# Optimization experiments

Measured on AMD Instinct MI355X. Metric: run time of the kernel, lower is better.

## Reference

```python
import jax, jax.numpy as jnp
import numpy as np

T = 32        # time_step
H = 64        # n_hidden (and dense width)
A = 8         # nb_actions
OBS_DIM = 512
B = 4096      # sequences; obs rows = B*T
LN_EPS = 1e-12  # tf.contrib.layers.layer_norm epsilon


def setup_inputs() -> dict:
    key = jax.random.key(0)
    ks = jax.random.split(key, 10)
    s = 0.1
    return {
        "obs":  jax.random.normal(ks[0], (B * T, OBS_DIM), jnp.float32),
        "W0":   jax.random.normal(ks[1], (OBS_DIM, H), jnp.float32) * s,
        "b0":   jnp.zeros((H,), jnp.float32),
        "gamma": jnp.ones((H,), jnp.float32),
        "beta":  jnp.zeros((H,), jnp.float32),
        "Wfw":  jax.random.normal(ks[2], (2 * H, 4 * H), jnp.float32) * s,
        "bfw":  jnp.zeros((4 * H,), jnp.float32),
        "Wbw":  jax.random.normal(ks[3], (2 * H, 4 * H), jnp.float32) * s,
        "bbw":  jnp.zeros((4 * H,), jnp.float32),
        "Wc":   jax.random.uniform(ks[4], (H, A), jnp.float32, -0.003, 0.003),
        "bc":   jnp.zeros((A,), jnp.float32),
    }


def _lstm_scan(xs, W, b):
    """BasicLSTMCell (forget_bias=1.0). xs: [T, B, H] -> hs: [T, B, H]."""
    nb = xs.shape[1]
    init = (jnp.zeros((nb, H), xs.dtype), jnp.zeros((nb, H), xs.dtype))

    def step(carry, x_t):
        c, h = carry
        z = jnp.concatenate([x_t, h], axis=-1) @ W + b  # [B, 4H]
        i, j, f, o = jnp.split(z, 4, axis=-1)           # TF gate order i,j,f,o
        c = c * jax.nn.sigmoid(f + 1.0) + jax.nn.sigmoid(i) * jnp.tanh(j)
        h = jnp.tanh(c) * jax.nn.sigmoid(o)
        return (c, h), h

    _, hs = jax.lax.scan(step, init, xs)
    return hs


def reference(obs, W0, b0, gamma, beta, Wfw, bfw, Wbw, bbw, Wc, bc):
    # dense(64) + layer_norm + relu
    x = obs @ W0 + b0                                   # [B*T, H]
    mu = jnp.mean(x, axis=-1, keepdims=True)
    var = jnp.mean(jnp.square(x - mu), axis=-1, keepdims=True)
    x = gamma * (x - mu) / jnp.sqrt(var + LN_EPS) + beta
    x = jax.nn.relu(x)

    xt = x.reshape(-1, T, H).transpose(1, 0, 2)          # [T, B, H]
    hs_fw = _lstm_scan(xt, Wfw, bfw)                     # [T, B, H]
    hs_bw = _lstm_scan(xt[::-1], Wbw, bbw)[::-1]         # reverse-in, reverse-out

    # tf.reshape on the (fw, bw) tuple stacks along a new leading axis:
    # [2, B, T, H] -> [2B, T*H, 1]; conv1d(kernel=stride=H) == per-step proj.
    y = jnp.stack([hs_fw.transpose(1, 0, 2), hs_bw.transpose(1, 0, 2)], axis=0)
    y = y.reshape(-1, T, H)                              # [2B, T, H]
    out = jnp.tanh(jnp.einsum('btk,ka->bta', y, Wc) + bc)  # [2B, T, A]
    return out
```

## Files before the change

### kernel.cpp

```cpp
#include <hip/hip_runtime.h>
#include <hip/hip_bf16.h>

typedef __attribute__((ext_vector_type(8))) short bf16x8;
typedef __attribute__((ext_vector_type(4))) float f32x4;

#define MFMA_BF16 __builtin_amdgcn_mfma_f32_16x16x32_bf16

#define GLDS16(gp, lp)                                                        \
  __builtin_amdgcn_global_load_lds(                                           \
      (const __attribute__((address_space(1))) void*)(gp),                    \
      (__attribute__((address_space(3))) void*)(lp), 16, 0, 0)

__device__ __forceinline__ unsigned pk2(float a, float b) {
  __hip_bfloat162 t = __float22bfloat162_rn(make_float2(a, b));
  return *reinterpret_cast<unsigned*>(&t);
}
__device__ __forceinline__ unsigned short f2bf_hw(float f) {
  __hip_bfloat16 h = __float2bfloat16(f);
  return *reinterpret_cast<unsigned short*>(&h);
}

__global__ void k0_conv(const float* __restrict__ W0, const float* __restrict__ Wfw,
                        const float* __restrict__ Wbw, unsigned short* __restrict__ wfrag,
                        unsigned short* __restrict__ wlstm) {
  int gid = blockIdx.x * 256 + threadIdx.x;
  if (gid < 4096) {
    int f = gid >> 6, l = gid & 63;
    int k0 = (f >> 2) * 32 + ((l >> 4) << 3);
    int n = (f & 3) * 16 + (l & 15);
    bf16x8 v;
#pragma unroll
    for (int j = 0; j < 8; ++j) v[j] = (short)f2bf_hw(W0[(k0 + j) * 64 + n]);
    *(bf16x8*)(wfrag + gid * 8) = v;
  } else if (gid < 12288) {
    int g2 = gid - 4096;
    const float* W = (g2 < 4096) ? Wfw : Wbw;
    int f = (g2 & 4095) >> 6, l = g2 & 63;
    int wv = f >> 4, gate = (f >> 2) & 3, kf = f & 3;
    int col = gate * 64 + wv * 16 + (l & 15);
    int kr = kf * 32 + ((l >> 4) << 3);
    bf16x8 v;
#pragma unroll
    for (int j = 0; j < 8; ++j) v[j] = (short)f2bf_hw(W[(kr + j) * 256 + col]);
    *(bf16x8*)(wlstm + g2 * 8) = v;
  }
}

__global__ __launch_bounds__(256, 3) void k_dense_ln(
    const float* __restrict__ obs, const unsigned short* __restrict__ wfrag,
    const float* __restrict__ b0, const float* __restrict__ gam,
    const float* __restrict__ bet, unsigned short* __restrict__ xout) {
  __shared__ __align__(16) char lds[49152];
  const int tid = threadIdx.x, w = tid >> 6, l = tid & 63;
  const int g = l >> 4, c = l & 15;
  const long blk64 = (long)blockIdx.x * 64;
  const long rb = blk64 + w * 16;

  float b0v[4], gv[4], bv[4];
#pragma unroll
  for (int nt = 0; nt < 4; ++nt) {
    int col = nt * 16 + c;
    b0v[nt] = b0[col]; gv[nt] = gam[col]; bv[nt] = bet[col];
  }
  const unsigned short* wfl = wfrag + l * 8;
  const char* gB = (const char*)obs + blk64 * 2048;

  const int rlo = w * 4 + g;
  asm volatile("s_waitcnt vmcnt(0)" ::: "memory");

#define K1_STAGE(q)                                                           \
  {                                                                           \
    _Pragma("unroll") for (int i = 0; i < 4; ++i) {                           \
      int row_ = i * 16 + rlo;                                                \
      const char* gp_ = gB + (long)row_ * 2048 + (q) * 256 +                  \
                        (long)((c ^ rlo) * 16);                               \
      char* lp_ = lds + ((q) % 3) * 16384 + (i * 4096 + (w * 64 + l) * 16);   \
      GLDS16(gp_, lp_);                                                       \
    }                                                                         \
  }

  K1_STAGE(0);
  K1_STAGE(1);
  K1_STAGE(2);

  f32x4 acc[4];
#pragma unroll
  for (int nt = 0; nt < 4; ++nt) acc[nt] = (f32x4){0.f, 0.f, 0.f, 0.f};

#pragma unroll
  for (int q = 0; q < 8; ++q) {
    constexpr int VW[8] = {8, 16, 24, 24, 24, 24, 20, 16};
    asm volatile("s_waitcnt vmcnt(%0)" :: "i"(VW[q]) : "memory");
    __builtin_amdgcn_s_barrier();
    __builtin_amdgcn_sched_barrier(0);

    const char* rowb = lds + (q % 3) * 16384 + (w * 16 + c) * 256;
#pragma unroll
    for (int kf = 0; kf < 2; ++kf) {
      int fb = (q * 2 + kf) * 4;
      bf16x8 B0 = *(const bf16x8*)(wfl + (fb + 0) * 512);
      bf16x8 B1 = *(const bf16x8*)(wfl + (fb + 1) * 512);
      bf16x8 B2 = *(const bf16x8*)(wfl + (fb + 2) * 512);
      bf16x8 B3 = *(const bf16x8*)(wfl + (fb + 3) * 512);
      int u0 = kf * 8 + g * 2;
      float4 f0 = *(const float4*)(rowb + ((u0 + 0) ^ c) * 16);
      float4 f1 = *(const float4*)(rowb + ((u0 + 1) ^ c) * 16);
      union { bf16x8 v; unsigned u[4]; } af;
      af.u[0] = pk2(f0.x, f0.y); af.u[1] = pk2(f0.z, f0.w);
      af.u[2] = pk2(f1.x, f1.y); af.u[3] = pk2(f1.z, f1.w);
      acc[0] = MFMA_BF16(af.v, B0, acc[0], 0, 0, 0);
      acc[1] = MFMA_BF16(af.v, B1, acc[1], 0, 0, 0);
      acc[2] = MFMA_BF16(af.v, B2, acc[2], 0, 0, 0);
      acc[3] = MFMA_BF16(af.v, B3, acc[3], 0, 0, 0);
    }
    if (q < 5) {
      __builtin_amdgcn_s_barrier();
      __builtin_amdgcn_sched_barrier(0);
      K1_STAGE(q + 3);
    }
  }

  float vv[4][4], s1[4], s2[4];
#pragma unroll
  for (int r = 0; r < 4; ++r) { s1[r] = 0.f; s2[r] = 0.f; }
#pragma unroll
  for (int nt = 0; nt < 4; ++nt)
#pragma unroll
    for (int r = 0; r < 4; ++r) {
      float val = acc[nt][r] + b0v[nt];
      vv[nt][r] = val; s1[r] += val; s2[r] += val * val;
    }
#pragma unroll
  for (int r = 0; r < 4; ++r) {
#pragma unroll
    for (int m = 1; m <= 8; m <<= 1) {
      s1[r] += __shfl_xor(s1[r], m);
      s2[r] += __shfl_xor(s2[r], m);
    }
  }
  unsigned short* xw = (unsigned short*)lds + w * 1024;
#pragma unroll
  for (int r = 0; r < 4; ++r) {
    float mu = s1[r] * 0.015625f;
    float var = s2[r] * 0.015625f - mu * mu;
    float inv = rsqrtf(var + 1e-12f);
    int row = g * 4 + r;
#pragma unroll
    for (int nt = 0; nt < 4; ++nt) {
      float xn = (vv[nt][r] - mu) * inv * gv[nt] + bv[nt];
      xw[(row * 64 + nt * 16 + c) ^ (g << 3)] = f2bf_hw(fmaxf(xn, 0.f));
    }
  }
#pragma unroll
  for (int m2 = 0; m2 < 2; ++m2) {
    int m = m2 * 64 + l;
    int row = m >> 3, u8 = m & 7;
    bf16x8 v = *(const bf16x8*)(xw + ((row * 64 + u8 * 8) ^ ((row >> 2) << 3)));
    *(bf16x8*)(xout + (rb + row) * 64 + u8 * 8) = v;
  }
}

__global__ __launch_bounds__(256, 2) void k_lstm(
    const unsigned short* __restrict__ x, const unsigned short* __restrict__ wlstm,
    const float* __restrict__ bfw, const float* __restrict__ bbw,
    const float* __restrict__ Wc, const float* __restrict__ bc,
    float* __restrict__ out) {
  __shared__ __align__(16) char xl[65536];
  __shared__ unsigned short hl[2 * 1024];
  const int tid = threadIdx.x, w = tid >> 6, l = tid & 63;
  const int g = l >> 4, c = l & 15;
  const int dir = blockIdx.x >> 8;
  const int sq = (blockIdx.x & 255) * 16;
  const float* bias = dir ? bbw : bfw;

  bf16x8 Bf[4][4];
  const unsigned short* wl = wlstm + ((long)dir * 4096 + w * 16 * 64) * 8;
#pragma unroll
  for (int gate = 0; gate < 4; ++gate)
#pragma unroll
    for (int kf = 0; kf < 4; ++kf)
      Bf[gate][kf] = *(const bf16x8*)(wl + ((gate * 4 + kf) * 64 + l) * 8);
  float bz[4];
#pragma unroll
  for (int gate = 0; gate < 4; ++gate) bz[gate] = bias[gate * 64 + w * 16 + c];

  bf16x8 Pc[2];
#pragma unroll
  for (int kf = 0; kf < 2; ++kf)
#pragma unroll
    for (int j = 0; j < 8; ++j) Pc[kf][j] = 0;
  float bcv = 0.f;
  if (w == 0 && c < 8) {
#pragma unroll
    for (int kf = 0; kf < 2; ++kf)
#pragma unroll
      for (int j = 0; j < 8; ++j)
        Pc[kf][j] = (short)f2bf_hw(Wc[(kf * 32 + g * 8 + j) * 8 + c]);
    bcv = bc[c];
  }

  asm volatile("s_waitcnt vmcnt(0)" ::: "memory");

  const int ss = l >> 3, sc = l & 7;
#pragma unroll
  for (int j = 0; j < 8; ++j) {
    int tt = w * 8 + j;
    int te = dir ? 31 - tt : tt;
#pragma unroll
    for (int p = 0; p < 2; ++p) {
      int s = p * 8 + ss;
      const char* gp = (const char*)x +
          ((long)(sq + s) * 32 + te) * 128 + (long)(sc ^ (s & 7)) * 16;
      char* lp = xl + tt * 2048 + p * 1024;
      GLDS16(gp, lp);
    }
  }

  for (int i = tid; i < 1024; i += 256) ((unsigned*)hl)[i] = 0u;
  float cs[4] = {0.f, 0.f, 0.f, 0.f};

  if (w == 0) asm volatile("s_waitcnt vmcnt(12)" ::: "memory");
  asm volatile("s_waitcnt lgkmcnt(0)" ::: "memory");
  __builtin_amdgcn_s_barrier();
  __builtin_amdgcn_sched_barrier(0);

  const int hq = w >> 1;
  const int hgp = ((w & 1) * 2 + (c >> 3)) * 16;
  const int hlo = c & 7;

  f32x4 accx[4];
  {
    const char* xt = xl + 0 * 2048 + c * 128;
    bf16x8 Ax0 = *(const bf16x8*)(xt + (long)((g) ^ (c & 7)) * 16);
    bf16x8 Ax1 = *(const bf16x8*)(xt + (long)((4 + g) ^ (c & 7)) * 16);
#pragma unroll
    for (int gate = 0; gate < 4; ++gate) {
      f32x4 b = (f32x4){bz[gate], bz[gate], bz[gate], bz[gate]};
      accx[gate] = MFMA_BF16(Ax1, Bf[gate][1],
                             MFMA_BF16(Ax0, Bf[gate][0], b, 0, 0, 0), 0, 0, 0);
    }
  }

  int p = 0;
#pragma unroll
  for (int t = 0; t < 32; ++t) {
    bf16x8 Ah0 = *(const bf16x8*)((const char*)hl + p * 2048 + l * 16);
    bf16x8 Ah1 = *(const bf16x8*)((const char*)hl + p * 2048 + 1024 + l * 16);

    f32x4 acc[4];
#pragma unroll
    for (int gate = 0; gate < 4; ++gate)
      acc[gate] = MFMA_BF16(Ah1, Bf[gate][3],
                            MFMA_BF16(Ah0, Bf[gate][2], accx[gate], 0, 0, 0),
                            0, 0, 0);

    if (t + 1 < 32) {
      const char* xt = xl + (t + 1) * 2048 + c * 128;
      bf16x8 Ax0 = *(const bf16x8*)(xt + (long)((g) ^ (c & 7)) * 16);
      bf16x8 Ax1 = *(const bf16x8*)(xt + (long)((4 + g) ^ (c & 7)) * 16);
#pragma unroll
      for (int gate = 0; gate < 4; ++gate) {
        f32x4 b = (f32x4){bz[gate], bz[gate], bz[gate], bz[gate]};
        accx[gate] = MFMA_BF16(Ax1, Bf[gate][1],
                               MFMA_BF16(Ax0, Bf[gate][0], b, 0, 0, 0), 0, 0, 0);
      }
    }

    const int wb = (p ^ 1) * 1024;
#pragma unroll
    for (int r = 0; r < 4; ++r) {
      float ei = __expf(-acc[0][r]);
      float ej = __expf(2.f * acc[1][r]);
      float ef = __expf(-(acc[2][r] + 1.f));
      float eo = __expf(-acc[3][r]);
      float p12 = (1.f + ei) * (1.f + ej);
      float r3 = __builtin_amdgcn_rcpf(p12 * (1.f + ef));
      float it = (ej - 1.f) * (1.f + ef) * r3;
      float sf = p12 * r3;
      cs[r] = cs[r] * sf + it;
      float ec = __expf(2.f * cs[r]);
      float r2 = __builtin_amdgcn_rcpf((1.f + eo) * (1.f + ec));
      hl[wb + (hq * 64 + hgp + 4 * g + r) * 8 + hlo] =
          f2bf_hw((ec - 1.f) * r2);
    }

    if (t + 2 < 32) {
      if (w == ((t + 2) >> 3))
        asm volatile("s_waitcnt vmcnt(%0)" :: "i"(14 - 2 * ((t + 2) & 7)) : "memory");
    }
    asm volatile("s_waitcnt lgkmcnt(0)" ::: "memory");
    __builtin_amdgcn_s_barrier();
    __builtin_amdgcn_sched_barrier(0);

    if (w == 0 && t >= 1) {
      int te = dir ? 31 - t : t;
      f32x4 pa = (f32x4){0.f, 0.f, 0.f, 0.f};
      pa = MFMA_BF16(Ah0, Pc[0], pa, 0, 0, 0);
      pa = MFMA_BF16(Ah1, Pc[1], pa, 0, 0, 0);
      if (c < 8) {
        int tp = dir ? 32 - t : t - 1;
#pragma unroll
        for (int r = 0; r < 4; ++r) {
          long orow = (long)dir * 4096 + sq + 4 * g + r;
          out[(orow * 32 + tp) * 8 + c] = tanhf(pa[r] + bcv);
        }
      }
    }
    p ^= 1;
  }

  if (w == 0) {
    bf16x8 Ph0 = *(const bf16x8*)((const char*)hl + p * 2048 + l * 16);
    bf16x8 Ph1 = *(const bf16x8*)((const char*)hl + p * 2048 + 1024 + l * 16);
    f32x4 pa = (f32x4){0.f, 0.f, 0.f, 0.f};
    pa = MFMA_BF16(Ph0, Pc[0], pa, 0, 0, 0);
    pa = MFMA_BF16(Ph1, Pc[1], pa, 0, 0, 0);
    if (c < 8) {
      int tp = dir ? 0 : 31;
#pragma unroll
      for (int r = 0; r < 4; ++r) {
        long orow = (long)dir * 4096 + sq + 4 * g + r;
        out[(orow * 32 + tp) * 8 + c] = tanhf(pa[r] + bcv);
      }
    }
  }
}

extern "C" void kernel_launch(void* const* d_in, const int* in_sizes, int n_in,
                              void* d_out, int out_size, void* d_ws, size_t ws_size,
                              hipStream_t stream) {
  const float* obs = (const float*)d_in[0];
  const float* W0  = (const float*)d_in[1];
  const float* b0  = (const float*)d_in[2];
  const float* gam = (const float*)d_in[3];
  const float* bet = (const float*)d_in[4];
  const float* Wfw = (const float*)d_in[5];
  const float* bfw = (const float*)d_in[6];
  const float* Wbw = (const float*)d_in[7];
  const float* bbw = (const float*)d_in[8];
  const float* Wc  = (const float*)d_in[9];
  const float* bc  = (const float*)d_in[10];
  float* out = (float*)d_out;

  unsigned short* wfrag = (unsigned short*)d_ws;
  unsigned short* wlstm = wfrag + 4096 * 8;
  unsigned short* xbf   = wlstm + 8192 * 8;

  k0_conv<<<48, 256, 0, stream>>>(W0, Wfw, Wbw, wfrag, wlstm);
  k_dense_ln<<<2048, 256, 0, stream>>>(obs, wfrag, b0, gam, bet, xbf);
  k_lstm<<<512, 256, 0, stream>>>(xbf, wlstm, bfw, bbw, Wc, bc, out);
}
```

Measured before the change: 102.3 us.

## Ring-buffer LSTM input staging, spread output projection across warps, coalesce output stores

Replaces the 64KB all-timesteps LDS buffer with an 8-slot ring buffer that is refilled during the time loop by a rotating warp. This cuts LDS use and may raise occupancy. The per-step output projection now runs on all four warps, each handling one row group, and uses a fast exp-based tanh. Results are gathered in an LDS tile and written to global memory at the end with coalesced float4 stores. Partial unrolling and the in-loop prefetch add sync dependencies, and the vmcnt accounting becomes fragile.

```diff
diff --git a/kernel.cpp b/kernel.cpp
--- a/kernel.cpp
+++ b/kernel.cpp
@@ -18,6 +18,9 @@
 __device__ __forceinline__ unsigned short f2bf_hw(float f) {
   __hip_bfloat16 h = __float2bfloat16(f);
   return *reinterpret_cast<unsigned short*>(&h);
+}
+__device__ __forceinline__ float tanh_f(float x) {
+  return 1.f - 2.f * __builtin_amdgcn_rcpf(1.f + __expf(2.f * x));
 }
 
 __global__ void k0_conv(const float* __restrict__ W0, const float* __restrict__ Wfw,
@@ -165,8 +168,9 @@
     const float* __restrict__ bfw, const float* __restrict__ bbw,
     const float* __restrict__ Wc, const float* __restrict__ bc,
     float* __restrict__ out) {
-  __shared__ __align__(16) char xl[65536];
+  __shared__ __align__(16) char xr[8 * 2048];
   __shared__ unsigned short hl[2 * 1024];
+  __shared__ float pl[16 * 32 * 8];
   const int tid = threadIdx.x, w = tid >> 6, l = tid & 63;
   const int g = l >> 4, c = l & 15;
   const int dir = blockIdx.x >> 8;
@@ -190,7 +194,7 @@
 #pragma unroll
     for (int j = 0; j < 8; ++j) Pc[kf][j] = 0;
   float bcv = 0.f;
-  if (w == 0 && c < 8) {
+  if (c < 8) {
 #pragma unroll
     for (int kf = 0; kf < 2; ++kf)
 #pragma unroll
@@ -202,24 +206,25 @@
   asm volatile("s_waitcnt vmcnt(0)" ::: "memory");
 
   const int ss = l >> 3, sc = l & 7;
-#pragma unroll
-  for (int j = 0; j < 8; ++j) {
-    int tt = w * 8 + j;
-    int te = dir ? 31 - tt : tt;
-#pragma unroll
-    for (int p = 0; p < 2; ++p) {
-      int s = p * 8 + ss;
-      const char* gp = (const char*)x +
-          ((long)(sq + s) * 32 + te) * 128 + (long)(sc ^ (s & 7)) * 16;
-      char* lp = xl + tt * 2048 + p * 1024;
-      GLDS16(gp, lp);
-    }
-  }
+#define K2_STAGE(tt)                                                          \
+  {                                                                           \
+    int te_ = dir ? 31 - (tt) : (tt);                                         \
+    _Pragma("unroll") for (int p_ = 0; p_ < 2; ++p_) {                        \
+      int s_ = p_ * 8 + ss;                                                   \
+      const char* gp_ = (const char*)x +                                      \
+          ((long)(sq + s_) * 32 + te_) * 128 + (long)(sc ^ (s_ & 7)) * 16;    \
+      char* lp_ = xr + ((tt) & 7) * 2048 + p_ * 1024;                         \
+      GLDS16(gp_, lp_);                                                       \
+    }                                                                         \
+  }
+
+  K2_STAGE(w);
+  K2_STAGE(w + 4);
 
   for (int i = tid; i < 1024; i += 256) ((unsigned*)hl)[i] = 0u;
   float cs[4] = {0.f, 0.f, 0.f, 0.f};
 
-  if (w == 0) asm volatile("s_waitcnt vmcnt(12)" ::: "memory");
+  if (w < 2) asm volatile("s_waitcnt vmcnt(2)" ::: "memory");
   asm volatile("s_waitcnt lgkmcnt(0)" ::: "memory");
   __builtin_amdgcn_s_barrier();
   __builtin_amdgcn_sched_barrier(0);
@@ -230,7 +235,7 @@
 
   f32x4 accx[4];
   {
-    const char* xt = xl + 0 * 2048 + c * 128;
+    const char* xt = xr + c * 128;
     bf16x8 Ax0 = *(const bf16x8*)(xt + (long)((g) ^ (c & 7)) * 16);
     bf16x8 Ax1 = *(const bf16x8*)(xt + (long)((4 + g) ^ (c & 7)) * 16);
 #pragma unroll
@@ -242,7 +247,7 @@
   }
 
   int p = 0;
-#pragma unroll
+#pragma unroll 2
   for (int t = 0; t < 32; ++t) {
     bf16x8 Ah0 = *(const bf16x8*)((const char*)hl + p * 2048 + l * 16);
     bf16x8 Ah1 = *(const bf16x8*)((const char*)hl + p * 2048 + 1024 + l * 16);
@@ -255,7 +260,7 @@
                             0, 0, 0);
 
     if (t + 1 < 32) {
-      const char* xt = xl + (t + 1) * 2048 + c * 128;
+      const char* xt = xr + ((t + 1) & 7) * 2048 + c * 128;
       bf16x8 Ax0 = *(const bf16x8*)(xt + (long)((g) ^ (c & 7)) * 16);
       bf16x8 Ax1 = *(const bf16x8*)(xt + (long)((4 + g) ^ (c & 7)) * 16);
 #pragma unroll
@@ -280,49 +285,54 @@
       cs[r] = cs[r] * sf + it;
       float ec = __expf(2.f * cs[r]);
       float r2 = __builtin_amdgcn_rcpf((1.f + eo) * (1.f + ec));
-      hl[wb + (hq * 64 + hgp + 4 * g + r) * 8 + hlo] =
-          f2bf_hw((ec - 1.f) * r2);
-    }
-
-    if (t + 2 < 32) {
-      if (w == ((t + 2) >> 3))
-        asm volatile("s_waitcnt vmcnt(%0)" :: "i"(14 - 2 * ((t + 2) & 7)) : "memory");
-    }
+      hl[wb + (hq * 64 + hgp + 4 * g + r) * 8 + hlo] = f2bf_hw((ec - 1.f) * r2);
+    }
+
+    if (t + 8 < 32 && w == (t & 3)) K2_STAGE(t + 8);
+
+    if (t + 2 < 32 && w == ((t + 2) & 3))
+      asm volatile("s_waitcnt vmcnt(2)" ::: "memory");
     asm volatile("s_waitcnt lgkmcnt(0)" ::: "memory");
     __builtin_amdgcn_s_barrier();
     __builtin_amdgcn_sched_barrier(0);
 
-    if (w == 0 && t >= 1) {
-      int te = dir ? 31 - t : t;
+    if (t >= 1) {
       f32x4 pa = (f32x4){0.f, 0.f, 0.f, 0.f};
       pa = MFMA_BF16(Ah0, Pc[0], pa, 0, 0, 0);
       pa = MFMA_BF16(Ah1, Pc[1], pa, 0, 0, 0);
-      if (c < 8) {
+      if (g == w && c < 8) {
         int tp = dir ? 32 - t : t - 1;
 #pragma unroll
-        for (int r = 0; r < 4; ++r) {
-          long orow = (long)dir * 4096 + sq + 4 * g + r;
-          out[(orow * 32 + tp) * 8 + c] = tanhf(pa[r] + bcv);
-        }
+        for (int r = 0; r < 4; ++r)
+          pl[(4 * g + r) * 256 + tp * 8 + c] = tanh_f(pa[r] + bcv);
       }
     }
     p ^= 1;
   }
 
-  if (w == 0) {
+  {
     bf16x8 Ph0 = *(const bf16x8*)((const char*)hl + p * 2048 + l * 16);
     bf16x8 Ph1 = *(const bf16x8*)((const char*)hl + p * 2048 + 1024 + l * 16);
     f32x4 pa = (f32x4){0.f, 0.f, 0.f, 0.f};
     pa = MFMA_BF16(Ph0, Pc[0], pa, 0, 0, 0);
     pa = MFMA_BF16(Ph1, Pc[1], pa, 0, 0, 0);
-    if (c < 8) {
+    if (g == w && c < 8) {
       int tp = dir ? 0 : 31;
 #pragma unroll
-      for (int r = 0; r < 4; ++r) {
-        long orow = (long)dir * 4096 + sq + 4 * g + r;
-        out[(orow * 32 + tp) * 8 + c] = tanhf(pa[r] + bcv);
-      }
-    }
+      for (int r = 0; r < 4; ++r)
+        pl[(4 * g + r) * 256 + tp * 8 + c] = tanh_f(pa[r] + bcv);
+    }
+  }
+
+  asm volatile("s_waitcnt lgkmcnt(0)" ::: "memory");
+  __builtin_amdgcn_s_barrier();
+#pragma unroll
+  for (int i = 0; i < 4; ++i) {
+    int fi = tid + i * 256;
+    int s = fi >> 6, rem = fi & 63;
+    int t2 = rem >> 1, a4 = (rem & 1) * 4;
+    float4 v = *(const float4*)(pl + s * 256 + t2 * 8 + a4);
+    *(float4*)(out + ((long)(dir * 4096 + sq + s) * 32 + t2) * 8 + a4) = v;
   }
 }
 
```

New measurement: 104.1 us. About the same (+1.8%).

## Process two 64-row tiles per block in dense+layernorm kernel with continuous pipeline

Applied to the files above, without the earlier changes.

The dense+LN kernel now handles two consecutive 64-row tiles per workgroup, with half as many blocks. The triple-buffered LDS load pipeline runs across both tiles without draining between them, and tile-0 results are kept in registers until the end. This removes one pipeline fill/drain per tile and halves the per-block setup cost. In exchange it uses more registers for the held results and there are fewer blocks to spread across the CUs. It also adds an unused sigmoid helper and removes a dead variable in the LSTM kernel.

```diff
diff --git a/kernel.cpp b/kernel.cpp
--- a/kernel.cpp
+++ b/kernel.cpp
@@ -18,6 +18,9 @@
 __device__ __forceinline__ unsigned short f2bf_hw(float f) {
   __hip_bfloat16 h = __float2bfloat16(f);
   return *reinterpret_cast<unsigned short*>(&h);
+}
+__device__ __forceinline__ float sigm(float x) {
+  return __builtin_amdgcn_rcpf(1.f + __expf(-x));
 }
 
 __global__ void k0_conv(const float* __restrict__ W0, const float* __restrict__ Wfw,
@@ -53,8 +56,6 @@
   __shared__ __align__(16) char lds[49152];
   const int tid = threadIdx.x, w = tid >> 6, l = tid & 63;
   const int g = l >> 4, c = l & 15;
-  const long blk64 = (long)blockIdx.x * 64;
-  const long rb = blk64 + w * 16;
 
   float b0v[4], gv[4], bv[4];
 #pragma unroll
@@ -63,18 +64,18 @@
     b0v[nt] = b0[col]; gv[nt] = gam[col]; bv[nt] = bet[col];
   }
   const unsigned short* wfl = wfrag + l * 8;
-  const char* gB = (const char*)obs + blk64 * 2048;
-
+  const char* gB = (const char*)obs + (long)blockIdx.x * 262144;
   const int rlo = w * 4 + g;
+
   asm volatile("s_waitcnt vmcnt(0)" ::: "memory");
 
-#define K1_STAGE(q)                                                           \
+#define K1_STAGE(cc)                                                          \
   {                                                                           \
     _Pragma("unroll") for (int i = 0; i < 4; ++i) {                           \
       int row_ = i * 16 + rlo;                                                \
-      const char* gp_ = gB + (long)row_ * 2048 + (q) * 256 +                  \
-                        (long)((c ^ rlo) * 16);                               \
-      char* lp_ = lds + ((q) % 3) * 16384 + (i * 4096 + (w * 64 + l) * 16);   \
+      const char* gp_ = gB + ((cc) >> 3) * 131072 + (long)row_ * 2048 +       \
+                        ((cc) & 7) * 256 + (long)((c ^ rlo) * 16);            \
+      char* lp_ = lds + ((cc) % 3) * 16384 + (i * 4096 + (w * 64 + l) * 16);  \
       GLDS16(gp_, lp_);                                                       \
     }                                                                         \
   }
@@ -86,18 +87,20 @@
   f32x4 acc[4];
 #pragma unroll
   for (int nt = 0; nt < 4; ++nt) acc[nt] = (f32x4){0.f, 0.f, 0.f, 0.f};
-
-#pragma unroll
-  for (int q = 0; q < 8; ++q) {
-    constexpr int VW[8] = {8, 16, 24, 24, 24, 24, 20, 16};
-    asm volatile("s_waitcnt vmcnt(%0)" :: "i"(VW[q]) : "memory");
+  unsigned short hv[2][16];
+
+#pragma unroll
+  for (int qq = 0; qq < 16; ++qq) {
+    constexpr int VW[16] = {8, 16, 24, 24, 24, 24, 24, 24,
+                            24, 24, 24, 24, 24, 24, 20, 16};
+    asm volatile("s_waitcnt vmcnt(%0)" :: "i"(VW[qq]) : "memory");
     __builtin_amdgcn_s_barrier();
     __builtin_amdgcn_sched_barrier(0);
 
-    const char* rowb = lds + (q % 3) * 16384 + (w * 16 + c) * 256;
+    const char* rowb = lds + (qq % 3) * 16384 + (w * 16 + c) * 256;
 #pragma unroll
     for (int kf = 0; kf < 2; ++kf) {
-      int fb = (q * 2 + kf) * 4;
+      int fb = ((qq & 7) * 2 + kf) * 4;
       bf16x8 B0 = *(const bf16x8*)(wfl + (fb + 0) * 512);
       bf16x8 B1 = *(const bf16x8*)(wfl + (fb + 1) * 512);
       bf16x8 B2 = *(const bf16x8*)(wfl + (fb + 2) * 512);
@@ -113,50 +116,65 @@
       acc[2] = MFMA_BF16(af.v, B2, acc[2], 0, 0, 0);
       acc[3] = MFMA_BF16(af.v, B3, acc[3], 0, 0, 0);
     }
-    if (q < 5) {
+    if (qq < 13) {
       __builtin_amdgcn_s_barrier();
       __builtin_amdgcn_sched_barrier(0);
-      K1_STAGE(q + 3);
-    }
-  }
-
-  float vv[4][4], s1[4], s2[4];
-#pragma unroll
-  for (int r = 0; r < 4; ++r) { s1[r] = 0.f; s2[r] = 0.f; }
-#pragma unroll
-  for (int nt = 0; nt < 4; ++nt)
+      K1_STAGE(qq + 3);
+    }
+    if ((qq & 7) == 7) {
+      const int tile = qq >> 3;
+      float vv[4][4], s1[4], s2[4];
+#pragma unroll
+      for (int r = 0; r < 4; ++r) { s1[r] = 0.f; s2[r] = 0.f; }
+#pragma unroll
+      for (int nt = 0; nt < 4; ++nt)
+#pragma unroll
+        for (int r = 0; r < 4; ++r) {
+          float val = acc[nt][r] + b0v[nt];
+          vv[nt][r] = val; s1[r] += val; s2[r] += val * val;
+        }
+#pragma unroll
+      for (int r = 0; r < 4; ++r) {
+#pragma unroll
+        for (int m = 1; m <= 8; m <<= 1) {
+          s1[r] += __shfl_xor(s1[r], m);
+          s2[r] += __shfl_xor(s2[r], m);
+        }
+      }
+#pragma unroll
+      for (int r = 0; r < 4; ++r) {
+        float mu = s1[r] * 0.015625f;
+        float var = s2[r] * 0.015625f - mu * mu;
+        float inv = rsqrtf(var + 1e-12f);
+#pragma unroll
+        for (int nt = 0; nt < 4; ++nt) {
+          float xn = (vv[nt][r] - mu) * inv * gv[nt] + bv[nt];
+          hv[tile][r * 4 + nt] = f2bf_hw(fmaxf(xn, 0.f));
+        }
+      }
+#pragma unroll
+      for (int nt = 0; nt < 4; ++nt) acc[nt] = (f32x4){0.f, 0.f, 0.f, 0.f};
+    }
+  }
+
+  unsigned short* xw = (unsigned short*)(lds + 16384) + w * 1024;
+#pragma unroll
+  for (int tile = 0; tile < 2; ++tile) {
+    const long rbt = ((long)blockIdx.x * 2 + tile) * 64 + w * 16;
 #pragma unroll
     for (int r = 0; r < 4; ++r) {
-      float val = acc[nt][r] + b0v[nt];
-      vv[nt][r] = val; s1[r] += val; s2[r] += val * val;
-    }
-#pragma unroll
-  for (int r = 0; r < 4; ++r) {
-#pragma unroll
-    for (int m = 1; m <= 8; m <<= 1) {
-      s1[r] += __shfl_xor(s1[r], m);
-      s2[r] += __shfl_xor(s2[r], m);
-    }
-  }
-  unsigned short* xw = (unsigned short*)lds + w * 1024;
-#pragma unroll
-  for (int r = 0; r < 4; ++r) {
-    float mu = s1[r] * 0.015625f;
-    float var = s2[r] * 0.015625f - mu * mu;
-    float inv = rsqrtf(var + 1e-12f);
-    int row = g * 4 + r;
-#pragma unroll
-    for (int nt = 0; nt < 4; ++nt) {
-      float xn = (vv[nt][r] - mu) * inv * gv[nt] + bv[nt];
-      xw[(row * 64 + nt * 16 + c) ^ (g << 3)] = f2bf_hw(fmaxf(xn, 0.f));
-    }
-  }
-#pragma unroll
-  for (int m2 = 0; m2 < 2; ++m2) {
-    int m = m2 * 64 + l;
-    int row = m >> 3, u8 = m & 7;
-    bf16x8 v = *(const bf16x8*)(xw + ((row * 64 + u8 * 8) ^ ((row >> 2) << 3)));
-    *(bf16x8*)(xout + (rb + row) * 64 + u8 * 8) = v;
+      int row = g * 4 + r;
+#pragma unroll
+      for (int nt = 0; nt < 4; ++nt)
+        xw[(row * 64 + nt * 16 + c) ^ (g << 3)] = hv[tile][r * 4 + nt];
+    }
+#pragma unroll
+    for (int m2 = 0; m2 < 2; ++m2) {
+      int m = m2 * 64 + l;
+      int row = m >> 3, u8 = m & 7;
+      bf16x8 v = *(const bf16x8*)(xw + ((row * 64 + u8 * 8) ^ ((row >> 2) << 3)));
+      *(bf16x8*)(xout + (rbt + row) * 64 + u8 * 8) = v;
+    }
   }
 }
 
@@ -280,8 +298,7 @@
       cs[r] = cs[r] * sf + it;
       float ec = __expf(2.f * cs[r]);
       float r2 = __builtin_amdgcn_rcpf((1.f + eo) * (1.f + ec));
-      hl[wb + (hq * 64 + hgp + 4 * g + r) * 8 + hlo] =
-          f2bf_hw((ec - 1.f) * r2);
+      hl[wb + (hq * 64 + hgp + 4 * g + r) * 8 + hlo] = f2bf_hw((ec - 1.f) * r2);
     }
 
     if (t + 2 < 32) {
@@ -293,7 +310,6 @@
     __builtin_amdgcn_sched_barrier(0);
 
     if (w == 0 && t >= 1) {
-      int te = dir ? 31 - t : t;
       f32x4 pa = (f32x4){0.f, 0.f, 0.f, 0.f};
       pa = MFMA_BF16(Ah0, Pc[0], pa, 0, 0, 0);
       pa = MFMA_BF16(Ah1, Pc[1], pa, 0, 0, 0);
@@ -347,6 +363,6 @@
   unsigned short* xbf   = wlstm + 8192 * 8;
 
   k0_conv<<<48, 256, 0, stream>>>(W0, Wfw, Wbw, wfrag, wlstm);
-  k_dense_ln<<<2048, 256, 0, stream>>>(obs, wfrag, b0, gam, bet, xbf);
+  k_dense_ln<<<1024, 256, 0, stream>>>(obs, wfrag, b0, gam, bet, xbf);
   k_lstm<<<512, 256, 0, stream>>>(xbf, wlstm, bfw, bbw, Wc, bc, out);
 }
```

New measurement: 112.3 us. +9.8%, slower.

## Defer output projection to after the recurrence, storing h into the consumed x buffer

Applied to the files above, without the earlier changes.

Each step's hidden state is now also written into that step's slot of the LDS x buffer, which the recurrence has already consumed. The per-step projection that wave 0 ran inside the serial loop is removed. After the loop all waves compute the projection and output for their own 8 time steps, using a cheaper exp/rcp tanh. This takes work off the serial critical path and spreads it across waves, at the cost of an extra LDS store per step and an added barrier before the loop so the x buffer is fully read before it is overwritten.

```diff
diff --git a/kernel.cpp b/kernel.cpp
--- a/kernel.cpp
+++ b/kernel.cpp
@@ -18,6 +18,9 @@
 __device__ __forceinline__ unsigned short f2bf_hw(float f) {
   __hip_bfloat16 h = __float2bfloat16(f);
   return *reinterpret_cast<unsigned short*>(&h);
+}
+__device__ __forceinline__ float tanh_f(float x) {
+  return 1.f - 2.f * __builtin_amdgcn_rcpf(1.f + __expf(2.f * x));
 }
 
 __global__ void k0_conv(const float* __restrict__ W0, const float* __restrict__ Wfw,
@@ -190,7 +193,7 @@
 #pragma unroll
     for (int j = 0; j < 8; ++j) Pc[kf][j] = 0;
   float bcv = 0.f;
-  if (w == 0 && c < 8) {
+  if (c < 8) {
 #pragma unroll
     for (int kf = 0; kf < 2; ++kf)
 #pragma unroll
@@ -240,6 +243,9 @@
                              MFMA_BF16(Ax0, Bf[gate][0], b, 0, 0, 0), 0, 0, 0);
     }
   }
+  asm volatile("s_waitcnt lgkmcnt(0)" ::: "memory");
+  __builtin_amdgcn_s_barrier();
+  __builtin_amdgcn_sched_barrier(0);
 
   int p = 0;
 #pragma unroll
@@ -267,6 +273,7 @@
     }
 
     const int wb = (p ^ 1) * 1024;
+    unsigned short* xh = (unsigned short*)xl + t * 1024;
 #pragma unroll
     for (int r = 0; r < 4; ++r) {
       float ei = __expf(-acc[0][r]);
@@ -280,8 +287,10 @@
       cs[r] = cs[r] * sf + it;
       float ec = __expf(2.f * cs[r]);
       float r2 = __builtin_amdgcn_rcpf((1.f + eo) * (1.f + ec));
-      hl[wb + (hq * 64 + hgp + 4 * g + r) * 8 + hlo] =
-          f2bf_hw((ec - 1.f) * r2);
+      unsigned short hb = f2bf_hw((ec - 1.f) * r2);
+      int off = (hq * 64 + hgp + 4 * g + r) * 8 + hlo;
+      hl[wb + off] = hb;
+      xh[off] = hb;
     }
 
     if (t + 2 < 32) {
@@ -291,36 +300,24 @@
     asm volatile("s_waitcnt lgkmcnt(0)" ::: "memory");
     __builtin_amdgcn_s_barrier();
     __builtin_amdgcn_sched_barrier(0);
-
-    if (w == 0 && t >= 1) {
-      int te = dir ? 31 - t : t;
-      f32x4 pa = (f32x4){0.f, 0.f, 0.f, 0.f};
-      pa = MFMA_BF16(Ah0, Pc[0], pa, 0, 0, 0);
-      pa = MFMA_BF16(Ah1, Pc[1], pa, 0, 0, 0);
-      if (c < 8) {
-        int tp = dir ? 32 - t : t - 1;
-#pragma unroll
-        for (int r = 0; r < 4; ++r) {
-          long orow = (long)dir * 4096 + sq + 4 * g + r;
-          out[(orow * 32 + tp) * 8 + c] = tanhf(pa[r] + bcv);
-        }
-      }
-    }
     p ^= 1;
   }
 
-  if (w == 0) {
-    bf16x8 Ph0 = *(const bf16x8*)((const char*)hl + p * 2048 + l * 16);
-    bf16x8 Ph1 = *(const bf16x8*)((const char*)hl + p * 2048 + 1024 + l * 16);
+#pragma unroll
+  for (int j = 0; j < 8; ++j) {
+    int t = w * 8 + j;
+    const char* hb = xl + t * 2048;
+    bf16x8 Ph0 = *(const bf16x8*)(hb + l * 16);
+    bf16x8 Ph1 = *(const bf16x8*)(hb + 1024 + l * 16);
     f32x4 pa = (f32x4){0.f, 0.f, 0.f, 0.f};
     pa = MFMA_BF16(Ph0, Pc[0], pa, 0, 0, 0);
     pa = MFMA_BF16(Ph1, Pc[1], pa, 0, 0, 0);
     if (c < 8) {
-      int tp = dir ? 0 : 31;
+      int tp = dir ? 31 - t : t;
 #pragma unroll
       for (int r = 0; r < 4; ++r) {
         long orow = (long)dir * 4096 + sq + 4 * g + r;
-        out[(orow * 32 + tp) * 8 + c] = tanhf(pa[r] + bcv);
+        out[(orow * 32 + tp) * 8 + c] = tanh_f(pa[r] + bcv);
       }
     }
   }
```

Result: faster. 98.58 us (-3.6%).
